# Kernel tuning notes

Hardware: AMD Instinct MI355X
Metric: run time of the kernel (lower is better)

The kernel has to match this reference:

```python
import jax, jax.numpy as jnp
import numpy as np

SCALING = 32.0 / 16  # alpha / rank


def setup_inputs() -> dict:
    key = jax.random.key(0)
    k1, k2, k3, k4, k5 = jax.random.split(key, 5)
    B, S, IN, OUT, R = 4, 2048, 4096, 4096, 16
    x = jax.random.normal(k1, (B, S, IN), dtype=jnp.float32)
    weight = jax.random.normal(k2, (OUT, IN), dtype=jnp.float32) * 0.02
    lora_a_w = jax.random.normal(k3, (R, IN), dtype=jnp.float32) * 0.02
    lora_b_w = jax.random.normal(k4, (OUT, R), dtype=jnp.float32) * 0.02
    magnitude = jax.random.uniform(k5, (OUT,), dtype=jnp.float32) + 0.5
    return {"x": x, "weight": weight, "lora_a_w": lora_a_w,
            "lora_b_w": lora_b_w, "magnitude": magnitude}


def reference(x, weight, lora_a_w, lora_b_w, magnitude):
    # base linear: x @ W^T  -> [..., out_dim]
    base_out = jnp.einsum('bsi,oi->bso', x, weight)
    # low-rank path (dropout is identity at p=0.0)
    lora_out = jnp.einsum('bsr,or->bso', jnp.einsum('bsi,ri->bsr', x, lora_a_w), lora_b_w)
    # merged low-rank weight B @ A (torch uses an eye-matrix trick; direct matmul is equivalent)
    lora_weight = lora_b_w @ lora_a_w  # [out, in]
    # row-wise norm of adapted weight; detached in the original
    weight_norm = jax.lax.stop_gradient(
        jnp.linalg.norm(weight + SCALING * lora_weight, axis=1))  # [out]
    mag_norm_scale = (magnitude / weight_norm)[None, None, :]  # [1,1,out]
    dora_out = (mag_norm_scale - 1.0) * base_out + mag_norm_scale * lora_out * SCALING
    return dora_out + base_out
```

## Files before the change

kernel.cpp:

```cpp
#include <hip/hip_runtime.h>
#include <hip/hip_bf16.h>
#include <stdint.h>

#define M_DIM 8192
#define N_DIM 4096
#define K_DIM 4096
#define R_DIM 16

typedef __attribute__((ext_vector_type(8))) short bf16x8;
typedef __attribute__((ext_vector_type(4))) float f32x4;

__device__ __forceinline__ unsigned short f2bf(float f) {
  union { float f; unsigned int u; } v; v.f = f;
  unsigned int r = 0x7FFFu + ((v.u >> 16) & 1u);
  return (unsigned short)((v.u + r) >> 16);
}

__device__ __forceinline__ void gload16(const unsigned short* g, unsigned short* l) {
  __builtin_amdgcn_global_load_lds(
      (const __attribute__((address_space(1))) void*)g,
      (__attribute__((address_space(3))) void*)l,
      16, 0, 0);
}

__global__ void cast_x_kernel(const float4* __restrict__ in,
                              ushort4* __restrict__ out, int n4) {
  int i = blockIdx.x * 256 + threadIdx.x;
  if (i < n4) {
    float4 f = in[i];
    ushort4 o;
    o.x = f2bf(f.x); o.y = f2bf(f.y); o.z = f2bf(f.z); o.w = f2bf(f.w);
    out[i] = o;
  }
}

__global__ void prep_w_kernel(const float* __restrict__ W,
                              const float* __restrict__ Aw,
                              const float* __restrict__ Bw,
                              const float* __restrict__ mag,
                              unsigned short* __restrict__ wbf,
                              float* __restrict__ scale) {
  const int o = blockIdx.x;
  const int tid = threadIdx.x;
  __shared__ float Bo[R_DIM];
  __shared__ float red[4];
  if (tid < R_DIM) Bo[tid] = Bw[o * R_DIM + tid];
  __syncthreads();
  float ss = 0.f;
  const size_t rowoff = (size_t)o * K_DIM;
  for (int i = tid; i < K_DIM; i += 256) {
    float v = W[rowoff + i];
    float acc = 0.f;
    #pragma unroll
    for (int r = 0; r < R_DIM; ++r) acc += Bo[r] * Aw[r * K_DIM + i];
    v += 2.0f * acc;
    ss += v * v;
    wbf[rowoff + i] = f2bf(v);
  }
  #pragma unroll
  for (int off = 32; off > 0; off >>= 1) ss += __shfl_down(ss, off, 64);
  if ((tid & 63) == 0) red[tid >> 6] = ss;
  __syncthreads();
  if (tid == 0)
    scale[o] = mag[o] / sqrtf(red[0] + red[1] + red[2] + red[3]);
}

__global__ void __launch_bounds__(256)
dora_gemm(const unsigned short* __restrict__ A,
          const unsigned short* __restrict__ Bt,
          const float* __restrict__ scale,
          float* __restrict__ C) {
  __shared__ __align__(16) unsigned short As[128 * 32];
  __shared__ __align__(16) unsigned short Bs[128 * 32];
  const int tid  = threadIdx.x;
  const int lane = tid & 63;
  const int wave = tid >> 6;
  const int bM = blockIdx.y * 128;
  const int bN = blockIdx.x * 128;

  const int sr = lane >> 2;
  const int sc = (lane & 3) * 8;
  const unsigned short* pa0 = A  + (size_t)(bM + wave * 32 + sr) * K_DIM + sc;
  const unsigned short* pa1 = pa0 + (size_t)16 * K_DIM;
  const unsigned short* pb0 = Bt + (size_t)(bN + wave * 32 + sr) * K_DIM + sc;
  const unsigned short* pb1 = pb0 + (size_t)16 * K_DIM;
  unsigned short* lA0 = &As[wave * 32 * 32];
  unsigned short* lA1 = lA0 + 16 * 32;
  unsigned short* lB0 = &Bs[wave * 32 * 32];
  unsigned short* lB1 = lB0 + 16 * 32;

  const int fr = lane & 15;
  const int fq = lane >> 4;
  const int wM = (wave >> 1) * 64;
  const int wN = (wave & 1) * 64;

  f32x4 acc[4][4];
  #pragma unroll
  for (int i = 0; i < 4; ++i)
    #pragma unroll
    for (int j = 0; j < 4; ++j) acc[i][j] = (f32x4){0.f, 0.f, 0.f, 0.f};

  for (int k0 = 0; k0 < K_DIM; k0 += 32) {
    gload16(pa0 + k0, lA0);
    gload16(pa1 + k0, lA1);
    gload16(pb0 + k0, lB0);
    gload16(pb1 + k0, lB1);
    __syncthreads();
    bf16x8 aF[4], bF[4];
    #pragma unroll
    for (int mt = 0; mt < 4; ++mt)
      aF[mt] = *(const bf16x8*)&As[(wM + mt * 16 + fr) * 32 + fq * 8];
    #pragma unroll
    for (int nt = 0; nt < 4; ++nt)
      bF[nt] = *(const bf16x8*)&Bs[(wN + nt * 16 + fr) * 32 + fq * 8];
    #pragma unroll
    for (int mt = 0; mt < 4; ++mt)
      #pragma unroll
      for (int nt = 0; nt < 4; ++nt)
        acc[mt][nt] = __builtin_amdgcn_mfma_f32_16x16x32_bf16(aF[mt], bF[nt], acc[mt][nt], 0, 0, 0);
    __syncthreads();
  }

  float scv[4];
  #pragma unroll
  for (int nt = 0; nt < 4; ++nt) scv[nt] = scale[bN + wN + nt * 16 + fr];
  #pragma unroll
  for (int mt = 0; mt < 4; ++mt) {
    const int m0 = bM + wM + mt * 16 + fq * 4;
    #pragma unroll
    for (int nt = 0; nt < 4; ++nt) {
      const int n = bN + wN + nt * 16 + fr;
      #pragma unroll
      for (int r = 0; r < 4; ++r)
        C[(size_t)(m0 + r) * N_DIM + n] = acc[mt][nt][r] * scv[nt];
    }
  }
}

extern "C" void kernel_launch(void* const* d_in, const int* in_sizes, int n_in,
                              void* d_out, int out_size, void* d_ws, size_t ws_size,
                              hipStream_t stream) {
  const float* x   = (const float*)d_in[0];
  const float* W   = (const float*)d_in[1];
  const float* la  = (const float*)d_in[2];
  const float* lb  = (const float*)d_in[3];
  const float* mag = (const float*)d_in[4];
  float* out = (float*)d_out;

  unsigned short* xbf = (unsigned short*)d_ws;
  unsigned short* wbf = (unsigned short*)((char*)d_ws + (size_t)M_DIM * K_DIM * 2);
  float* scale = (float*)((char*)d_ws + (size_t)M_DIM * K_DIM * 2 + (size_t)N_DIM * K_DIM * 2);

  const int n4 = (M_DIM * K_DIM) / 4;
  cast_x_kernel<<<(n4 + 255) / 256, 256, 0, stream>>>((const float4*)x, (ushort4*)xbf, n4);
  prep_w_kernel<<<N_DIM, 256, 0, stream>>>(W, la, lb, mag, wbf, scale);
  dim3 grid(N_DIM / 128, M_DIM / 128);
  dora_gemm<<<grid, 256, 0, stream>>>(xbf, wbf, scale, out);
}
```

Before: 622.0 us.

## Fuse x cast and weight prep into one kernel, swizzle GEMM LDS layout

Merges the x-to-bf16 cast and the merged-weight/norm prep into a single launch. Weight blocks now handle 16 output rows each and stage a chunk of lora_a in shared memory, so lora_a is reused across rows and loads are vectorised. The GEMM also XOR-swizzles the 16-byte column slot in LDS on both the global-to-LDS write and the fragment read, to cut bank conflicts. The 64KB of LDS in the prep blocks lowers their occupancy, and the swizzle has to match exactly on both sides to stay correct.

```diff
diff --git a/kernel.cpp b/kernel.cpp
--- a/kernel.cpp
+++ b/kernel.cpp
@@ -6,6 +6,9 @@
 #define N_DIM 4096
 #define K_DIM 4096
 #define R_DIM 16
+
+#define PREP_BLOCKS 256
+#define CAST_BLOCKS 8192
 
 typedef __attribute__((ext_vector_type(8))) short bf16x8;
 typedef __attribute__((ext_vector_type(4))) float f32x4;
@@ -23,46 +26,83 @@
       16, 0, 0);
 }
 
-__global__ void cast_x_kernel(const float4* __restrict__ in,
-                              ushort4* __restrict__ out, int n4) {
-  int i = blockIdx.x * 256 + threadIdx.x;
-  if (i < n4) {
-    float4 f = in[i];
-    ushort4 o;
-    o.x = f2bf(f.x); o.y = f2bf(f.y); o.z = f2bf(f.z); o.w = f2bf(f.w);
-    out[i] = o;
-  }
-}
-
-__global__ void prep_w_kernel(const float* __restrict__ W,
-                              const float* __restrict__ Aw,
-                              const float* __restrict__ Bw,
-                              const float* __restrict__ mag,
-                              unsigned short* __restrict__ wbf,
-                              float* __restrict__ scale) {
-  const int o = blockIdx.x;
+__global__ void __launch_bounds__(256) prep_kernel(
+    const float4* __restrict__ x4, ushort4* __restrict__ xbf4,
+    const float* __restrict__ W, const float* __restrict__ Aw,
+    const float* __restrict__ Bw, const float* __restrict__ mag,
+    unsigned short* __restrict__ wbf, float* __restrict__ scale) {
   const int tid = threadIdx.x;
-  __shared__ float Bo[R_DIM];
-  __shared__ float red[4];
-  if (tid < R_DIM) Bo[tid] = Bw[o * R_DIM + tid];
+
+  if (blockIdx.x >= PREP_BLOCKS) {
+    const int base = (blockIdx.x - PREP_BLOCKS) * 1024 + tid;
+    #pragma unroll
+    for (int u = 0; u < 4; ++u) {
+      const int i = base + u * 256;
+      float4 f = x4[i];
+      ushort4 o;
+      o.x = f2bf(f.x); o.y = f2bf(f.y); o.z = f2bf(f.z); o.w = f2bf(f.w);
+      xbf4[i] = o;
+    }
+    return;
+  }
+
+  __shared__ float AwS[16 * 1024];
+  __shared__ float BoS[16 * 16];
+  __shared__ float red[16 * 4];
+  const int o0 = blockIdx.x * 16;
+
+  BoS[tid] = Bw[(o0 + (tid >> 4)) * R_DIM + (tid & 15)];
+
+  float ss[16];
+  #pragma unroll
+  for (int i = 0; i < 16; ++i) ss[i] = 0.f;
+
+  const float4* W4  = (const float4*)W;
+  const float4* Aw4 = (const float4*)Aw;
+  ushort4* wbf4 = (ushort4*)wbf;
+
+  for (int c = 0; c < 4; ++c) {
+    __syncthreads();
+    #pragma unroll
+    for (int t = tid; t < 4096; t += 256) {
+      const int r  = t >> 8;
+      const int j4 = t & 255;
+      ((float4*)AwS)[r * 256 + j4] = Aw4[(size_t)r * 1024 + c * 256 + j4];
+    }
+    __syncthreads();
+    #pragma unroll 4
+    for (int i = 0; i < 16; ++i) {
+      float4 w = W4[((size_t)(o0 + i) * K_DIM + c * 1024) / 4 + tid];
+      float4 acc = {0.f, 0.f, 0.f, 0.f};
+      #pragma unroll
+      for (int r = 0; r < R_DIM; ++r) {
+        const float b = BoS[i * 16 + r];
+        const float4 a = ((const float4*)AwS)[r * 256 + tid];
+        acc.x += b * a.x; acc.y += b * a.y; acc.z += b * a.z; acc.w += b * a.w;
+      }
+      float4 v;
+      v.x = w.x + 2.f * acc.x; v.y = w.y + 2.f * acc.y;
+      v.z = w.z + 2.f * acc.z; v.w = w.w + 2.f * acc.w;
+      ss[i] += v.x * v.x + v.y * v.y + v.z * v.z + v.w * v.w;
+      ushort4 o;
+      o.x = f2bf(v.x); o.y = f2bf(v.y); o.z = f2bf(v.z); o.w = f2bf(v.w);
+      wbf4[((size_t)(o0 + i) * K_DIM + c * 1024) / 4 + tid] = o;
+    }
+  }
+
+  const int lane = tid & 63, wave = tid >> 6;
+  #pragma unroll
+  for (int i = 0; i < 16; ++i) {
+    float s = ss[i];
+    #pragma unroll
+    for (int off = 32; off > 0; off >>= 1) s += __shfl_down(s, off, 64);
+    if (lane == 0) red[i * 4 + wave] = s;
+  }
   __syncthreads();
-  float ss = 0.f;
-  const size_t rowoff = (size_t)o * K_DIM;
-  for (int i = tid; i < K_DIM; i += 256) {
-    float v = W[rowoff + i];
-    float acc = 0.f;
-    #pragma unroll
-    for (int r = 0; r < R_DIM; ++r) acc += Bo[r] * Aw[r * K_DIM + i];
-    v += 2.0f * acc;
-    ss += v * v;
-    wbf[rowoff + i] = f2bf(v);
-  }
-  #pragma unroll
-  for (int off = 32; off > 0; off >>= 1) ss += __shfl_down(ss, off, 64);
-  if ((tid & 63) == 0) red[tid >> 6] = ss;
-  __syncthreads();
-  if (tid == 0)
-    scale[o] = mag[o] / sqrtf(red[0] + red[1] + red[2] + red[3]);
+  if (tid < 16) {
+    const float s = red[tid * 4] + red[tid * 4 + 1] + red[tid * 4 + 2] + red[tid * 4 + 3];
+    scale[o0 + tid] = mag[o0 + tid] / sqrtf(s);
+  }
 }
 
 __global__ void __launch_bounds__(256)
@@ -79,7 +119,7 @@
   const int bN = blockIdx.x * 128;
 
   const int sr = lane >> 2;
-  const int sc = (lane & 3) * 8;
+  const int sc = (((lane & 3) ^ ((lane >> 3) & 3)) * 8);
   const unsigned short* pa0 = A  + (size_t)(bM + wave * 32 + sr) * K_DIM + sc;
   const unsigned short* pa1 = pa0 + (size_t)16 * K_DIM;
   const unsigned short* pb0 = Bt + (size_t)(bN + wave * 32 + sr) * K_DIM + sc;
@@ -91,6 +131,8 @@
 
   const int fr = lane & 15;
   const int fq = lane >> 4;
+  const int xr = (fr >> 1) & 3;
+  const int cA = (fq ^ xr) * 8;
   const int wM = (wave >> 1) * 64;
   const int wN = (wave & 1) * 64;
 
@@ -109,10 +151,10 @@
     bf16x8 aF[4], bF[4];
     #pragma unroll
     for (int mt = 0; mt < 4; ++mt)
-      aF[mt] = *(const bf16x8*)&As[(wM + mt * 16 + fr) * 32 + fq * 8];
+      aF[mt] = *(const bf16x8*)&As[(wM + mt * 16 + fr) * 32 + cA];
     #pragma unroll
     for (int nt = 0; nt < 4; ++nt)
-      bF[nt] = *(const bf16x8*)&Bs[(wN + nt * 16 + fr) * 32 + fq * 8];
+      bF[nt] = *(const bf16x8*)&Bs[(wN + nt * 16 + fr) * 32 + cA];
     #pragma unroll
     for (int mt = 0; mt < 4; ++mt)
       #pragma unroll
@@ -151,9 +193,8 @@
   unsigned short* wbf = (unsigned short*)((char*)d_ws + (size_t)M_DIM * K_DIM * 2);
   float* scale = (float*)((char*)d_ws + (size_t)M_DIM * K_DIM * 2 + (size_t)N_DIM * K_DIM * 2);
 
-  const int n4 = (M_DIM * K_DIM) / 4;
-  cast_x_kernel<<<(n4 + 255) / 256, 256, 0, stream>>>((const float4*)x, (ushort4*)xbf, n4);
-  prep_w_kernel<<<N_DIM, 256, 0, stream>>>(W, la, lb, mag, wbf, scale);
+  prep_kernel<<<PREP_BLOCKS + CAST_BLOCKS, 256, 0, stream>>>(
+      (const float4*)x, (ushort4*)xbf, W, la, lb, mag, wbf, scale);
   dim3 grid(N_DIM / 128, M_DIM / 128);
   dora_gemm<<<grid, 256, 0, stream>>>(xbf, wbf, scale, out);
 }
```

New measurement: 595.2 us. 1.05x faster.
